# Kernel optimization log

Measured on AMD Instinct MI355X. Metric: run time of the kernel, lower is better.

## Reference

```python
import jax, jax.numpy as jnp
import numpy as np

KERNEL_MUL = 2.0
KERNEL_NUM = 5


def setup_inputs() -> dict:
    key = jax.random.key(0)
    k1, k2 = jax.random.split(key)
    source = jax.random.normal(k1, (4096, 512), dtype=jnp.float32)
    target = jax.random.normal(k2, (4096, 512), dtype=jnp.float32)
    return {"source": source, "target": target}


def reference(source, target):
    b = source.shape[0]
    total = jnp.concatenate([source, target], axis=0)  # [N, D]
    n = total.shape[0]
    # pairwise squared L2 via dot-product trick (same math as expand-subtract)
    sq = jnp.sum(total * total, axis=1)  # [N]
    L2 = sq[:, None] + sq[None, :] - 2.0 * (total @ total.T)  # [N, N]
    # bandwidth uses .data in torch -> constant w.r.t. grads
    bw = jax.lax.stop_gradient(jnp.sum(L2)) / (n * n - n)
    bw = bw / (KERNEL_MUL ** (KERNEL_NUM // 2))
    kernels = jnp.zeros_like(L2)
    for i in range(KERNEL_NUM):  # small fixed loop over bandwidths
        kernels = kernels + jnp.exp(-L2 / (bw * (KERNEL_MUL ** i)))
    XX = jnp.mean(kernels[:b, :b])
    YY = jnp.mean(kernels[b:, b:])
    XY = jnp.mean(kernels[:b, b:])
    YX = jnp.mean(kernels[b:, :b])
    return XX + YY - XY - YX
```

## Files before the change

kernel.cpp:

```cpp
#include <hip/hip_runtime.h>
#include <cstdint>
#include <cstddef>


#define D_DIM 512
#define B_ROWS 4096
#define N_ROWS 8192
#define NTILES 64
#define NBLK_MMD 2080
#define LDS_HALF 8192
#define LDS_BUF 16384
#define QPITCH 528

typedef __attribute__((ext_vector_type(4))) int i32x4;

__device__ inline float waveReduce(float v) {
    #pragma unroll
    for (int off = 32; off > 0; off >>= 1) v += __shfl_down(v, off, 64);
    return v;
}

__device__ inline int q8(float x) {
    int v = (int)rintf(x * 16.f);
    v = v > 127 ? 127 : v;
    v = v < -127 ? -127 : v;
    return v & 255;
}


__global__ __launch_bounds__(256) void k_rowstats(const float* __restrict__ src,
                                                  const float* __restrict__ tgt,
                                                  unsigned char* __restrict__ Tp,
                                                  float* __restrict__ sq,
                                                  int* __restrict__ partial,
                                                  unsigned int* __restrict__ tk) {
    if (blockIdx.x == 0 && threadIdx.x < 65)
        tk[threadIdx.x * 16] = 0u;

    __shared__ unsigned char Q[16 * QPITCH];
    int tid = threadIdx.x, wave = tid >> 6, lane = tid & 63;
    int rb = blockIdx.x;

    #pragma unroll
    for (int i = 0; i < 4; ++i) {
        int rl  = wave * 4 + i;
        int row = rb * 16 + rl;
        const float* base = (row < B_ROWS) ? (src + (size_t)row * D_DIM)
                                           : (tgt + (size_t)(row - B_ROWS) * D_DIM);
        float4 a = ((const float4*)base)[lane * 2];
        float4 b = ((const float4*)base)[lane * 2 + 1];
        uint2 o;
        o.x = (unsigned)(q8(a.x) | (q8(a.y) << 8) | (q8(a.z) << 16) | (q8(a.w) << 24));
        o.y = (unsigned)(q8(b.x) | (q8(b.y) << 8) | (q8(b.z) << 16) | (q8(b.w) << 24));
        *(uint2*)(Q + rl * QPITCH + lane * 8) = o;
        float s = a.x*a.x + a.y*a.y + a.z*a.z + a.w*a.w
                + b.x*b.x + b.y*b.y + b.z*b.z + b.w*b.w;
        s = waveReduce(s);
        if (lane == 0) sq[row] = s;
    }
    __syncthreads();

    int s0 = 0, s1 = 0;
    #pragma unroll
    for (int r = 0; r < 16; ++r) {
        unsigned short v = *(const unsigned short*)(Q + r * QPITCH + tid * 2);
        s0 += (int)(signed char)(v & 255);
        s1 += (int)(signed char)(v >> 8);
    }
    int2 pv; pv.x = s0; pv.y = s1;
    *(int2*)(partial + (size_t)rb * 512 + tid * 2) = pv;

    int c = tid >> 3, idx = tid & 7;
    uint4 lo = *(const uint4*)(Q + (idx * 2)     * QPITCH + c * 16);
    uint4 hi = *(const uint4*)(Q + (idx * 2 + 1) * QPITCH + c * 16);
    unsigned char* gout = Tp + ((size_t)rb << 13) + c * 256 + idx * 32;
    *(uint4*)(gout)      = lo;
    *(uint4*)(gout + 16) = hi;
}

__global__ __launch_bounds__(512) void k_bw(const int* __restrict__ partial,
                                            const float* __restrict__ sq,
                                            float* __restrict__ c16out) {
    int t = threadIdx.x;
    int csum = 0;
    #pragma unroll 8
    for (int i = 0; i < 512; ++i) csum += partial[i * 512 + t];
    float cs = (float)csum * 0.0625f;
    float p = cs * cs;
    float ssq = 0.f;
    #pragma unroll
    for (int i = 0; i < 16; ++i) ssq += sq[t + i * 512];
    __shared__ float r8[8], q8s[8];
    float wp = waveReduce(p);
    float wq = waveReduce(ssq);
    if ((t & 63) == 0) { r8[t >> 6] = wp; q8s[t >> 6] = wq; }
    __syncthreads();
    if (t == 0) {
        double P = 0.0, Q = 0.0;
        #pragma unroll
        for (int i = 0; i < 8; ++i) { P += r8[i]; Q += q8s[i]; }
        double n = (double)N_ROWS;
        double sumL2 = 2.0 * n * Q - 2.0 * P;
        double bw = sumL2 / (n * n - n) / 4.0;
        c16out[0] = (float)(-1.4426950408889634 / (16.0 * bw));
    }
}

__global__ __launch_bounds__(256) void k_mmd(const unsigned char* __restrict__ Tp,
                                             const float* __restrict__ sq,
                                             const float* __restrict__ c16in,
                                             float* __restrict__ blockpart,
                                             float* __restrict__ out,
                                             unsigned int* __restrict__ tk) {
    int hwbid = (int)blockIdx.x;
    int bid = (hwbid & 7) * 260 + (hwbid >> 3);

    int rem = bid;
    int ti = 0, rowlen = NTILES;
    while (rem >= rowlen) { rem -= rowlen; rowlen--; ti++; }
    int tj = ti + rem;

    int tid  = threadIdx.x;
    int wave = tid >> 6;
    int lane = tid & 63;
    int waveM = (wave >> 1) * 64;
    int waveN = (wave & 1) * 64;
    int l15   = lane & 15;
    int quad  = lane >> 4;

    float c16 = c16in[0];
    float cgq = -2.f * c16 * (1.f / 256.f);

    int rbA0 = ti * 8;
    int rbB0 = tj * 8;

    __shared__ unsigned char lds[2 * LDS_BUF];

    i32x4 acc[4][4];
    #pragma unroll
    for (int mi = 0; mi < 4; ++mi)
        #pragma unroll
        for (int ni = 0; ni < 4; ++ni)
            acc[mi][ni] = (i32x4){0, 0, 0, 0};

    auto stage = [&](int buf, int kk) {
        unsigned char* lbase = lds + buf * LDS_BUF;
        #pragma unroll
        for (int s = 0; s < 2; ++s) {
            int rbl = wave * 2 + s;
            const unsigned char* gA =
                Tp + (((size_t)((rbA0 + rbl) * 32 + kk * 4)) << 8) + lane * 16;
            const unsigned char* gB =
                Tp + (((size_t)((rbB0 + rbl) * 32 + kk * 4)) << 8) + lane * 16;
            __builtin_amdgcn_global_load_lds(
                (const __attribute__((address_space(1))) void*)gA,
                (__attribute__((address_space(3))) void*)(lbase + rbl * 1024 + lane * 16),
                16, 0, 0);
            __builtin_amdgcn_global_load_lds(
                (const __attribute__((address_space(1))) void*)gB,
                (__attribute__((address_space(3))) void*)(lbase + LDS_HALF + rbl * 1024 + lane * 16),
                16, 0, 0);
        }
    };

    stage(0, 0);
    __syncthreads();

    int aoff = ((wave >> 1) * 4) * 1024 + quad * 256 + l15 * 16;
    int boff = ((wave & 1) * 4) * 1024 + quad * 256 + l15 * 16;

    int buf = 0;
    for (int kk = 0; kk < 8; ++kk) {
        if (kk < 7) stage(buf ^ 1, kk + 1);

        const unsigned char* bufA = lds + buf * LDS_BUF;
        const unsigned char* bufB = bufA + LDS_HALF;
        i32x4 af[4], bf[4];
        #pragma unroll
        for (int mi = 0; mi < 4; ++mi)
            af[mi] = *(const i32x4*)(bufA + aoff + mi * 1024);
        #pragma unroll
        for (int ni = 0; ni < 4; ++ni)
            bf[ni] = *(const i32x4*)(bufB + boff + ni * 1024);
        #pragma unroll
        for (int mi = 0; mi < 4; ++mi)
            #pragma unroll
            for (int ni = 0; ni < 4; ++ni)
                acc[mi][ni] = __builtin_amdgcn_mfma_i32_16x16x64_i8(
                    af[mi], bf[ni], acc[mi][ni], 0, 0, 0);

        __syncthreads();
        buf ^= 1;
    }

    const float* sqA = sq + ti * 128;
    const float* sqB = sq + tj * 128;
    float trow16[16];
    #pragma unroll
    for (int mi = 0; mi < 4; ++mi)
        #pragma unroll
        for (int r = 0; r < 4; ++r)
            trow16[mi * 4 + r] = sqA[waveM + mi * 16 + quad * 4 + r] * c16;
    float tcol16[4];
    #pragma unroll
    for (int ni = 0; ni < 4; ++ni)
        tcol16[ni] = sqB[waveN + ni * 16 + l15] * c16;

    float psum = 0.f;
    if (ti != tj) {
        #pragma unroll
        for (int mi = 0; mi < 4; ++mi) {
            #pragma unroll
            for (int ni = 0; ni < 4; ++ni) {
                #pragma unroll
                for (int r = 0; r < 4; ++r) {
                    float g   = (float)acc[mi][ni][r];
                    float t16 = __builtin_fmaf(g, cgq, trow16[mi * 4 + r]) + tcol16[ni];
                    float e1  = __builtin_amdgcn_exp2f(t16);
                    float e2  = e1 * e1;
                    float e4  = e2 * e2;
                    float e8  = e4 * e4;
                    float e16 = e8 * e8;
                    psum += ((e1 + e2) + (e4 + e8)) + e16;
                }
            }
        }
    } else {
        #pragma unroll
        for (int mi = 0; mi < 4; ++mi) {
            #pragma unroll
            for (int ni = 0; ni < 4; ++ni) {
                #pragma unroll
                for (int r = 0; r < 4; ++r) {
                    float g   = (float)acc[mi][ni][r];
                    float t16 = __builtin_fmaf(g, cgq, trow16[mi * 4 + r]) + tcol16[ni];
                    float e1  = __builtin_amdgcn_exp2f(t16);
                    float e2  = e1 * e1;
                    float e4  = e2 * e2;
                    float e8  = e4 * e4;
                    float e16 = e8 * e8;
                    float ks5 = ((e1 + e2) + (e4 + e8)) + e16;
                    int rl = waveM + mi * 16 + quad * 4 + r;
                    int cl = waveN + ni * 16 + l15;
                    psum += (rl == cl) ? 5.0f : ks5;
                }
            }
        }
    }

    float* red = (float*)lds;
    __shared__ bool isLast;
    float w = waveReduce(psum);
    if (lane == 0) red[wave] = w;
    __syncthreads();
    if (tid == 0) {
        float tot   = red[0] + red[1] + red[2] + red[3];
        float sign  = ((ti < 32) == (tj < 32)) ? 1.f : -1.f;
        float scale = (ti == tj) ? sign : 2.f * sign;
        __hip_atomic_store(&blockpart[hwbid], tot * scale,
                           __ATOMIC_RELAXED, __HIP_MEMORY_SCOPE_AGENT);
        asm volatile("s_waitcnt vmcnt(0)" ::: "memory");
        unsigned g = (unsigned)hwbid & 63u;
        unsigned tgt = (g < 32u) ? 33u : 32u;
        unsigned prev = __hip_atomic_fetch_add(&tk[g * 16], 1u,
                            __ATOMIC_RELAXED, __HIP_MEMORY_SCOPE_AGENT);
        bool last = false;
        if (prev == tgt - 1u)
            last = (__hip_atomic_fetch_add(&tk[64 * 16], 1u,
                        __ATOMIC_RELAXED, __HIP_MEMORY_SCOPE_AGENT) == 63u);
        isLast = last;
    }
    __syncthreads();
    if (!isLast) return;

    float s = 0.f;
    for (int i = tid; i < NBLK_MMD; i += 256)
        s += __hip_atomic_load(&blockpart[i], __ATOMIC_RELAXED,
                               __HIP_MEMORY_SCOPE_AGENT);
    float ws = waveReduce(s);
    if (lane == 0) red[wave] = ws;
    __syncthreads();
    if (tid == 0)
        out[0] = (red[0] + red[1] + red[2] + red[3]) * (1.f / (4096.f * 4096.f));
}

extern "C" void kernel_launch(void* const* d_in, const int* in_sizes, int n_in,
                              void* d_out, int out_size, void* d_ws, size_t ws_size,
                              hipStream_t stream) {
    const float* src = (const float*)d_in[0];
    const float* tgt = (const float*)d_in[1];

    uint8_t* ws = (uint8_t*)d_ws;
    unsigned char* Tp = (unsigned char*)ws;
    size_t off = 4194304;
    float* sq      = (float*)(ws + off); off += 32768;
    int*   partial = (int*)  (ws + off); off += 512 * 512 * 4;
    float* bp      = (float*)(ws + off); off += 8320;
    float* c16     = (float*)(ws + off); off += 64;
    unsigned int* tk = (unsigned int*)(ws + off);

    k_rowstats<<<512, 256, 0, stream>>>(src, tgt, Tp, sq, partial, tk);
    k_bw      <<<1, 512, 0, stream>>>(partial, sq, c16);
    k_mmd     <<<NBLK_MMD, 256, 0, stream>>>(Tp, sq, c16, bp, (float*)d_out, tk);
}
```

Baseline: 125.8 us.

## Load full K tiles into LDS at once and atomically pre-reduce column sums

The MMD kernel now loads the entire 128x512 int8 A and B tiles (128 KB of LDS) in one shot with a single barrier, replacing the double-buffered per-k staging loop and its per-iteration syncs. Column partial sums in rowstats are atomically accumulated into 8 groups, so the single-block bandwidth kernel reads 8 rows instead of 512; this adds a memset launch. The large LDS footprint limits occupancy to one block per CU and removes overlap of loads with MFMA work.

```diff
diff --git a/kernel.cpp b/kernel.cpp
--- a/kernel.cpp
+++ b/kernel.cpp
@@ -8,8 +8,6 @@
 #define N_ROWS 8192
 #define NTILES 64
 #define NBLK_MMD 2080
-#define LDS_HALF 8192
-#define LDS_BUF 16384
 #define QPITCH 528
 
 typedef __attribute__((ext_vector_type(4))) int i32x4;
@@ -27,12 +25,11 @@
     return v & 255;
 }
 
-
 __global__ __launch_bounds__(256) void k_rowstats(const float* __restrict__ src,
                                                   const float* __restrict__ tgt,
                                                   unsigned char* __restrict__ Tp,
                                                   float* __restrict__ sq,
-                                                  int* __restrict__ partial,
+                                                  int* __restrict__ sp,
                                                   unsigned int* __restrict__ tk) {
     if (blockIdx.x == 0 && threadIdx.x < 65)
         tk[threadIdx.x * 16] = 0u;
@@ -67,8 +64,9 @@
         s0 += (int)(signed char)(v & 255);
         s1 += (int)(signed char)(v >> 8);
     }
-    int2 pv; pv.x = s0; pv.y = s1;
-    *(int2*)(partial + (size_t)rb * 512 + tid * 2) = pv;
+    int gbase = (rb & 7) * 512 + tid * 2;
+    atomicAdd(&sp[gbase],     s0);
+    atomicAdd(&sp[gbase + 1], s1);
 
     int c = tid >> 3, idx = tid & 7;
     uint4 lo = *(const uint4*)(Q + (idx * 2)     * QPITCH + c * 16);
@@ -78,13 +76,13 @@
     *(uint4*)(gout + 16) = hi;
 }
 
-__global__ __launch_bounds__(512) void k_bw(const int* __restrict__ partial,
+__global__ __launch_bounds__(512) void k_bw(const int* __restrict__ sp,
                                             const float* __restrict__ sq,
                                             float* __restrict__ c16out) {
     int t = threadIdx.x;
     int csum = 0;
-    #pragma unroll 8
-    for (int i = 0; i < 512; ++i) csum += partial[i * 512 + t];
+    #pragma unroll
+    for (int g = 0; g < 8; ++g) csum += sp[g * 512 + t];
     float cs = (float)csum * 0.0625f;
     float p = cs * cs;
     float ssq = 0.f;
@@ -131,10 +129,22 @@
     float c16 = c16in[0];
     float cgq = -2.f * c16 * (1.f / 256.f);
 
-    int rbA0 = ti * 8;
-    int rbB0 = tj * 8;
-
-    __shared__ unsigned char lds[2 * LDS_BUF];
+    __shared__ unsigned char lds[131072];
+    unsigned char* ldsA = lds;
+    unsigned char* ldsB = lds + 65536;
+    const unsigned char* gA = Tp + ((size_t)ti << 16);
+    const unsigned char* gB = Tp + ((size_t)tj << 16);
+    #pragma unroll
+    for (int i = 0; i < 16; ++i) {
+        int o = (i * 256 + tid) * 16;
+        __builtin_amdgcn_global_load_lds(
+            (const __attribute__((address_space(1))) void*)(gA + o),
+            (__attribute__((address_space(3))) void*)(ldsA + o), 16, 0, 0);
+        __builtin_amdgcn_global_load_lds(
+            (const __attribute__((address_space(1))) void*)(gB + o),
+            (__attribute__((address_space(3))) void*)(ldsB + o), 16, 0, 0);
+    }
+    __syncthreads();
 
     i32x4 acc[4][4];
     #pragma unroll
@@ -143,54 +153,24 @@
         for (int ni = 0; ni < 4; ++ni)
             acc[mi][ni] = (i32x4){0, 0, 0, 0};
 
-    auto stage = [&](int buf, int kk) {
-        unsigned char* lbase = lds + buf * LDS_BUF;
-        #pragma unroll
-        for (int s = 0; s < 2; ++s) {
-            int rbl = wave * 2 + s;
-            const unsigned char* gA =
-                Tp + (((size_t)((rbA0 + rbl) * 32 + kk * 4)) << 8) + lane * 16;
-            const unsigned char* gB =
-                Tp + (((size_t)((rbB0 + rbl) * 32 + kk * 4)) << 8) + lane * 16;
-            __builtin_amdgcn_global_load_lds(
-                (const __attribute__((address_space(1))) void*)gA,
-                (__attribute__((address_space(3))) void*)(lbase + rbl * 1024 + lane * 16),
-                16, 0, 0);
-            __builtin_amdgcn_global_load_lds(
-                (const __attribute__((address_space(1))) void*)gB,
-                (__attribute__((address_space(3))) void*)(lbase + LDS_HALF + rbl * 1024 + lane * 16),
-                16, 0, 0);
-        }
-    };
-
-    stage(0, 0);
-    __syncthreads();
-
-    int aoff = ((wave >> 1) * 4) * 1024 + quad * 256 + l15 * 16;
-    int boff = ((wave & 1) * 4) * 1024 + quad * 256 + l15 * 16;
-
-    int buf = 0;
+    int arow = (wave >> 1) * 4;
+    int brow = (wave & 1) * 4;
+    #pragma unroll
     for (int kk = 0; kk < 8; ++kk) {
-        if (kk < 7) stage(buf ^ 1, kk + 1);
-
-        const unsigned char* bufA = lds + buf * LDS_BUF;
-        const unsigned char* bufB = bufA + LDS_HALF;
+        int coff = (kk * 4 + quad) * 256 + l15 * 16;
         i32x4 af[4], bf[4];
         #pragma unroll
         for (int mi = 0; mi < 4; ++mi)
-            af[mi] = *(const i32x4*)(bufA + aoff + mi * 1024);
+            af[mi] = *(const i32x4*)(ldsA + (arow + mi) * 8192 + coff);
         #pragma unroll
         for (int ni = 0; ni < 4; ++ni)
-            bf[ni] = *(const i32x4*)(bufB + boff + ni * 1024);
+            bf[ni] = *(const i32x4*)(ldsB + (brow + ni) * 8192 + coff);
         #pragma unroll
         for (int mi = 0; mi < 4; ++mi)
             #pragma unroll
             for (int ni = 0; ni < 4; ++ni)
                 acc[mi][ni] = __builtin_amdgcn_mfma_i32_16x16x64_i8(
                     af[mi], bf[ni], acc[mi][ni], 0, 0, 0);
-
-        __syncthreads();
-        buf ^= 1;
     }
 
     const float* sqA = sq + ti * 128;
@@ -248,8 +228,9 @@
         }
     }
 
-    float* red = (float*)lds;
-    __shared__ bool isLast;
+    __syncthreads();
+    float* red   = (float*)lds;
+    int*   flagp = (int*)lds + 4;
     float w = waveReduce(psum);
     if (lane == 0) red[wave] = w;
     __syncthreads();
@@ -264,20 +245,21 @@
         unsigned tgt = (g < 32u) ? 33u : 32u;
         unsigned prev = __hip_atomic_fetch_add(&tk[g * 16], 1u,
                             __ATOMIC_RELAXED, __HIP_MEMORY_SCOPE_AGENT);
-        bool last = false;
+        int last = 0;
         if (prev == tgt - 1u)
             last = (__hip_atomic_fetch_add(&tk[64 * 16], 1u,
                         __ATOMIC_RELAXED, __HIP_MEMORY_SCOPE_AGENT) == 63u);
-        isLast = last;
-    }
-    __syncthreads();
-    if (!isLast) return;
+        *flagp = last;
+    }
+    __syncthreads();
+    if (!*flagp) return;
 
     float s = 0.f;
     for (int i = tid; i < NBLK_MMD; i += 256)
         s += __hip_atomic_load(&blockpart[i], __ATOMIC_RELAXED,
                                __HIP_MEMORY_SCOPE_AGENT);
     float ws = waveReduce(s);
+    __syncthreads();
     if (lane == 0) red[wave] = ws;
     __syncthreads();
     if (tid == 0)
@@ -294,12 +276,13 @@
     unsigned char* Tp = (unsigned char*)ws;
     size_t off = 4194304;
     float* sq      = (float*)(ws + off); off += 32768;
-    int*   partial = (int*)  (ws + off); off += 512 * 512 * 4;
+    int*   sp      = (int*)  (ws + off); off += 16384;
     float* bp      = (float*)(ws + off); off += 8320;
     float* c16     = (float*)(ws + off); off += 64;
     unsigned int* tk = (unsigned int*)(ws + off);
 
-    k_rowstats<<<512, 256, 0, stream>>>(src, tgt, Tp, sq, partial, tk);
-    k_bw      <<<1, 512, 0, stream>>>(partial, sq, c16);
+    hipMemsetAsync(sp, 0, 16384, stream);
+    k_rowstats<<<512, 256, 0, stream>>>(src, tgt, Tp, sq, sp, tk);
+    k_bw      <<<1, 512, 0, stream>>>(sp, sq, c16);
     k_mmd     <<<NBLK_MMD, 256, 0, stream>>>(Tp, sq, c16, bp, (float*)d_out, tk);
 }
```

After: 132.2 us. 5.1% more time.
